# Optimization experiments

Hardware: AMD Instinct MI355X
Metric: run time of the kernel (lower is better)

Reference implementation:

```python
import jax, jax.numpy as jnp
import numpy as np

B, NELEC, NATOMS, SH_PER_ATOM, NORB, NCTR = 512, 100, 20, 30, 300, 2
NBAS = NATOMS * SH_PER_ATOM  # 600 == NORB * NCTR


def _ipow(x, k):
    # x**k for integer k in {0,1,2}; safe for negative x (cartesian harmonics)
    return jnp.where(k == 0, jnp.ones_like(x), jnp.where(k == 1, x, x * x))


def setup_inputs() -> dict:
    key = jax.random.key(0)
    ks = jax.random.split(key, 7)
    pos = jax.random.normal(ks[0], (B, NELEC * 3), jnp.float32)
    atom_coords = jax.random.normal(ks[1], (NATOMS, 3), jnp.float32)
    bas_exp = jax.random.uniform(ks[2], (NBAS,), jnp.float32, 0.5, 3.0)
    bas_n = jax.random.randint(ks[3], (NBAS,), 0, 3).astype(jnp.float32)
    norm_cst = jax.random.uniform(ks[4], (NBAS,), jnp.float32, 0.5, 1.5)
    bas_coeffs = jax.random.normal(ks[5], (NBAS,), jnp.float32)
    bas_kxyz = jax.random.randint(ks[6], (NBAS, 3), 0, 3)  # kx, ky, kz exponents
    index_ctr = jnp.repeat(jnp.arange(NORB, dtype=jnp.int32), NCTR)  # nbas -> norb
    return {"pos": pos, "atom_coords": atom_coords, "bas_exp": bas_exp,
            "bas_n": bas_n, "norm_cst": norm_cst, "bas_coeffs": bas_coeffs,
            "bas_kxyz": bas_kxyz, "index_ctr": index_ctr}


def reference(pos, atom_coords, bas_exp, bas_n, norm_cst, bas_coeffs, bas_kxyz, index_ctr):
    # gather: per-shell atom coordinates  (NBAS, 3)
    bas_coords = jnp.repeat(atom_coords, SH_PER_ATOM, axis=0)
    # electron - basis-center displacement  (B, Nelec, NBAS, 3)
    xyz = pos.reshape(-1, NELEC, 1, 3) - bas_coords[None, None]
    r2 = jnp.sum(xyz * xyz, axis=-1)                 # (B, Nelec, NBAS)
    r = jnp.sqrt(r2)
    # radial_gaussian: r^n * exp(-alpha r^2)
    R = jnp.power(r, bas_n) * jnp.exp(-bas_exp * r2)
    # cartesian harmonics: x^kx * y^ky * z^kz
    Y = (_ipow(xyz[..., 0], bas_kxyz[:, 0]) *
         _ipow(xyz[..., 1], bas_kxyz[:, 1]) *
         _ipow(xyz[..., 2], bas_kxyz[:, 2]))
    # ao kernel + contraction (segment-sum over basis fns into orbitals)
    vals = (norm_cst * bas_coeffs) * R * Y           # (B, Nelec, NBAS)
    ao = jnp.zeros((pos.shape[0], NELEC, NORB), vals.dtype).at[:, :, index_ctr].add(vals)
    return ao
```

## Files before the change

### kernel.cpp

```cpp
#include <hip/hip_runtime.h>

#define BATCH   512
#define NELEC   100
#define NATOMS  20
#define SH      30
#define NORB    300
#define NBAS    600
#define NROWS   (BATCH * NELEC)
#define RPT     8
#define NRG     (NROWS / RPT)
#define NTHREADS (NORB * NRG)

__device__ __forceinline__ float eval_basis(
    float px, float py, float pz,
    float ax, float ay, float az,
    float alpha, float n, float c,
    int kx, int ky, int kz)
{
    float dx = px - ax, dy = py - ay, dz = pz - az;
    float r2 = dx * dx + dy * dy + dz * dz;
    float r  = sqrtf(r2);
    float R = (n < 0.5f) ? 1.0f : ((n < 1.5f) ? r : r2);
    float e = __expf(-alpha * r2);
    float yx = (kx == 0) ? 1.0f : dx;  yx = (kx == 2) ? yx * dx : yx;
    float yy = (ky == 0) ? 1.0f : dy;  yy = (ky == 2) ? yy * dy : yy;
    float yz = (kz == 0) ? 1.0f : dz;  yz = (kz == 2) ? yz * dz : yz;
    return c * R * e * (yx * yy * yz);
}

__global__ __launch_bounds__(256) void ao_kernel(
    const float* __restrict__ pos,
    const float* __restrict__ atom_coords,
    const float* __restrict__ bas_exp,
    const float* __restrict__ bas_n,
    const float* __restrict__ norm_cst,
    const float* __restrict__ bas_coeffs,
    const int*   __restrict__ bas_kxyz,
    float*       __restrict__ out)
{
    int tid = blockIdx.x * blockDim.x + threadIdx.x;
    if (tid >= NTHREADS) return;
    int o  = tid % NORB;
    int rg = tid / NORB;

    int s0 = 2 * o, s1 = s0 + 1;

    float a0 = bas_exp[s0],  a1 = bas_exp[s1];
    float n0 = bas_n[s0],    n1 = bas_n[s1];
    float c0 = norm_cst[s0] * bas_coeffs[s0];
    float c1 = norm_cst[s1] * bas_coeffs[s1];
    int kx0 = bas_kxyz[3 * s0 + 0], ky0 = bas_kxyz[3 * s0 + 1], kz0 = bas_kxyz[3 * s0 + 2];
    int kx1 = bas_kxyz[3 * s1 + 0], ky1 = bas_kxyz[3 * s1 + 1], kz1 = bas_kxyz[3 * s1 + 2];
    int at0 = s0 / SH, at1 = s1 / SH;
    float ax0 = atom_coords[3 * at0 + 0], ay0 = atom_coords[3 * at0 + 1], az0 = atom_coords[3 * at0 + 2];
    float ax1 = atom_coords[3 * at1 + 0], ay1 = atom_coords[3 * at1 + 1], az1 = atom_coords[3 * at1 + 2];

    int row0 = rg * RPT;
#pragma unroll
    for (int r = 0; r < RPT; ++r) {
        int row = row0 + r;
        float px = pos[row * 3 + 0];
        float py = pos[row * 3 + 1];
        float pz = pos[row * 3 + 2];
        float v0 = eval_basis(px, py, pz, ax0, ay0, az0, a0, n0, c0, kx0, ky0, kz0);
        float v1 = eval_basis(px, py, pz, ax1, ay1, az1, a1, n1, c1, kx1, ky1, kz1);
        out[row * NORB + o] = v0 + v1;
    }
}

extern "C" void kernel_launch(void* const* d_in, const int* in_sizes, int n_in,
                              void* d_out, int out_size, void* d_ws, size_t ws_size,
                              hipStream_t stream) {
    const float* pos         = (const float*)d_in[0];
    const float* atom_coords = (const float*)d_in[1];
    const float* bas_exp     = (const float*)d_in[2];
    const float* bas_n       = (const float*)d_in[3];
    const float* norm_cst    = (const float*)d_in[4];
    const float* bas_coeffs  = (const float*)d_in[5];
    const int*   bas_kxyz    = (const int*)d_in[6];
    float* out = (float*)d_out;

    int blocks = (NTHREADS + 255) / 256;
    ao_kernel<<<blocks, 256, 0, stream>>>(pos, atom_coords, bas_exp, bas_n,
                                          norm_cst, bas_coeffs, bas_kxyz, out);
}
```

Before: 113.0 us.

## Restructure to one block per 64 rows with shared positions and exp2

Each block now handles 64 electron rows. Positions are staged in shared memory, and each of 300 active threads owns one orbital, computing its per-basis parameters once and looping over the rows. The exponent is pre-scaled by log2(e) so the loop can use exp2f. This amortizes parameter loads over more rows and shares the position loads across the block. It leaves 20 of 320 threads idle and produces fewer, longer blocks (800), which lowers parallelism per block.

```diff
diff --git a/kernel.cpp b/kernel.cpp
--- a/kernel.cpp
+++ b/kernel.cpp
@@ -7,28 +7,13 @@
 #define NORB    300
 #define NBAS    600
 #define NROWS   (BATCH * NELEC)
-#define RPT     8
-#define NRG     (NROWS / RPT)
-#define NTHREADS (NORB * NRG)
+#define ROWS    64
+#define NBLOCKS (NROWS / ROWS)
+#define BLOCK   320
 
-__device__ __forceinline__ float eval_basis(
-    float px, float py, float pz,
-    float ax, float ay, float az,
-    float alpha, float n, float c,
-    int kx, int ky, int kz)
-{
-    float dx = px - ax, dy = py - ay, dz = pz - az;
-    float r2 = dx * dx + dy * dy + dz * dz;
-    float r  = sqrtf(r2);
-    float R = (n < 0.5f) ? 1.0f : ((n < 1.5f) ? r : r2);
-    float e = __expf(-alpha * r2);
-    float yx = (kx == 0) ? 1.0f : dx;  yx = (kx == 2) ? yx * dx : yx;
-    float yy = (ky == 0) ? 1.0f : dy;  yy = (ky == 2) ? yy * dy : yy;
-    float yz = (kz == 0) ? 1.0f : dz;  yz = (kz == 2) ? yz * dz : yz;
-    return c * R * e * (yx * yy * yz);
-}
+#define LOG2E 1.4426950408889634f
 
-__global__ __launch_bounds__(256) void ao_kernel(
+__global__ __launch_bounds__(BLOCK) void ao_kernel(
     const float* __restrict__ pos,
     const float* __restrict__ atom_coords,
     const float* __restrict__ bas_exp,
@@ -38,33 +23,63 @@
     const int*   __restrict__ bas_kxyz,
     float*       __restrict__ out)
 {
-    int tid = blockIdx.x * blockDim.x + threadIdx.x;
-    if (tid >= NTHREADS) return;
-    int o  = tid % NORB;
-    int rg = tid / NORB;
+    __shared__ float spos[ROWS * 3];
 
-    int s0 = 2 * o, s1 = s0 + 1;
+    const int t    = threadIdx.x;
+    const int row0 = blockIdx.x * ROWS;
 
-    float a0 = bas_exp[s0],  a1 = bas_exp[s1];
-    float n0 = bas_n[s0],    n1 = bas_n[s1];
-    float c0 = norm_cst[s0] * bas_coeffs[s0];
-    float c1 = norm_cst[s1] * bas_coeffs[s1];
-    int kx0 = bas_kxyz[3 * s0 + 0], ky0 = bas_kxyz[3 * s0 + 1], kz0 = bas_kxyz[3 * s0 + 2];
-    int kx1 = bas_kxyz[3 * s1 + 0], ky1 = bas_kxyz[3 * s1 + 1], kz1 = bas_kxyz[3 * s1 + 2];
-    int at0 = s0 / SH, at1 = s1 / SH;
-    float ax0 = atom_coords[3 * at0 + 0], ay0 = atom_coords[3 * at0 + 1], az0 = atom_coords[3 * at0 + 2];
-    float ax1 = atom_coords[3 * at1 + 0], ay1 = atom_coords[3 * at1 + 1], az1 = atom_coords[3 * at1 + 2];
+    {
+        const float* src = pos + (size_t)row0 * 3;
+        for (int i = t; i < ROWS * 3; i += BLOCK) spos[i] = src[i];
+    }
+    __syncthreads();
 
-    int row0 = rg * RPT;
-#pragma unroll
-    for (int r = 0; r < RPT; ++r) {
-        int row = row0 + r;
-        float px = pos[row * 3 + 0];
-        float py = pos[row * 3 + 1];
-        float pz = pos[row * 3 + 2];
-        float v0 = eval_basis(px, py, pz, ax0, ay0, az0, a0, n0, c0, kx0, ky0, kz0);
-        float v1 = eval_basis(px, py, pz, ax1, ay1, az1, a1, n1, c1, kx1, ky1, kz1);
-        out[row * NORB + o] = v0 + v1;
+    if (t < NORB) {
+        const int s0 = 2 * t, s1 = s0 + 1;
+
+        const float al0 = bas_exp[s0] * LOG2E;
+        const float al1 = bas_exp[s1] * LOG2E;
+        const int   n0  = (int)bas_n[s0];
+        const int   n1  = (int)bas_n[s1];
+        const float c0  = norm_cst[s0] * bas_coeffs[s0];
+        const float c1  = norm_cst[s1] * bas_coeffs[s1];
+        const int  kx0 = bas_kxyz[3 * s0 + 0], ky0 = bas_kxyz[3 * s0 + 1], kz0 = bas_kxyz[3 * s0 + 2];
+        const int  kx1 = bas_kxyz[3 * s1 + 0], ky1 = bas_kxyz[3 * s1 + 1], kz1 = bas_kxyz[3 * s1 + 2];
+        const int  at0 = s0 / SH, at1 = s1 / SH;
+        const float ax0 = atom_coords[3 * at0 + 0], ay0 = atom_coords[3 * at0 + 1], az0 = atom_coords[3 * at0 + 2];
+        const float ax1 = atom_coords[3 * at1 + 0], ay1 = atom_coords[3 * at1 + 1], az1 = atom_coords[3 * at1 + 2];
+
+        float* op = out + (size_t)row0 * NORB + t;
+
+#pragma unroll 4
+        for (int r = 0; r < ROWS; ++r) {
+            const float px = spos[3 * r + 0];
+            const float py = spos[3 * r + 1];
+            const float pz = spos[3 * r + 2];
+
+            float dx = px - ax0, dy = py - ay0, dz = pz - az0;
+            float r2 = dx * dx + dy * dy + dz * dz;
+            float rr = sqrtf(r2);
+            float R  = (n0 == 0) ? 1.0f : ((n0 == 1) ? rr : r2);
+            float e  = exp2f(-al0 * r2);
+            float yx = (kx0 == 0) ? 1.0f : dx;  yx = (kx0 == 2) ? yx * dx : yx;
+            float yy = (ky0 == 0) ? 1.0f : dy;  yy = (ky0 == 2) ? yy * dy : yy;
+            float yz = (kz0 == 0) ? 1.0f : dz;  yz = (kz0 == 2) ? yz * dz : yz;
+            float v  = c0 * R * e * (yx * yy * yz);
+
+            dx = px - ax1; dy = py - ay1; dz = pz - az1;
+            r2 = dx * dx + dy * dy + dz * dz;
+            rr = sqrtf(r2);
+            R  = (n1 == 0) ? 1.0f : ((n1 == 1) ? rr : r2);
+            e  = exp2f(-al1 * r2);
+            yx = (kx1 == 0) ? 1.0f : dx;  yx = (kx1 == 2) ? yx * dx : yx;
+            yy = (ky1 == 0) ? 1.0f : dy;  yy = (ky1 == 2) ? yy * dy : yy;
+            yz = (kz1 == 0) ? 1.0f : dz;  yz = (kz1 == 2) ? yz * dz : yz;
+            v += c1 * R * e * (yx * yy * yz);
+
+            *op = v;
+            op += NORB;
+        }
     }
 }
 
@@ -80,7 +95,6 @@
     const int*   bas_kxyz    = (const int*)d_in[6];
     float* out = (float*)d_out;
 
-    int blocks = (NTHREADS + 255) / 256;
-    ao_kernel<<<blocks, 256, 0, stream>>>(pos, atom_coords, bas_exp, bas_n,
-                                          norm_cst, bas_coeffs, bas_kxyz, out);
+    ao_kernel<<<NBLOCKS, BLOCK, 0, stream>>>(pos, atom_coords, bas_exp, bas_n,
+                                             norm_cst, bas_coeffs, bas_kxyz, out);
 }
```

Result: slower. 123.6 us (+9.3%).
